# Optimization experiments

Measured on AMD Instinct MI355X. Metric: run time of the kernel, lower is better.

Reference implementation:

```python
import jax, jax.numpy as jnp
import numpy as np

N_NODES = 50000
N_EDGES = 400000
N_GRAPHS = 64
D_IN = 256
D_HID = 256
D_OUT = 16


def _gcn_conv(x, edge_index, W, b):
    """PyG-style GCNConv: h = D^{-1/2}(A+I)D^{-1/2} (x @ W) + b."""
    n = x.shape[0]
    loop = jnp.arange(n)
    src = jnp.concatenate([edge_index[0], loop])  # [E+N]
    dst = jnp.concatenate([edge_index[1], loop])
    deg = jax.ops.segment_sum(jnp.ones_like(dst, x.dtype), dst, num_segments=n)
    dinv = jnp.where(deg > 0, jax.lax.rsqrt(deg), jnp.zeros_like(deg))
    norm = dinv[src] * dinv[dst]  # [E+N]
    h = x @ W  # linear transform first (as PyG does)
    msg = h[src] * norm[:, None]  # gather + scale, [E+N, D]
    out = jax.ops.segment_sum(msg, dst, num_segments=n)  # scatter-add
    return out + b


def setup_inputs() -> dict:
    key = jax.random.key(0)
    ks = jax.random.split(key, 12)
    x = jax.random.normal(ks[0], (N_NODES, D_IN), dtype=jnp.float32)
    edge_index = jax.random.randint(ks[1], (2, N_EDGES), 0, N_NODES, dtype=jnp.int64)
    batch = jnp.sort(jax.random.randint(ks[2], (N_NODES,), 0, N_GRAPHS, dtype=jnp.int64))

    def glorot(k, fan_in, fan_out):
        s = np.sqrt(6.0 / (fan_in + fan_out)).astype(np.float32)
        return jax.random.uniform(k, (fan_in, fan_out), jnp.float32, -s, s)

    return {
        "x": x,
        "edge_index": edge_index,
        "batch": batch,
        "W1": glorot(ks[3], D_IN, D_HID), "b1": jnp.zeros((D_HID,), jnp.float32),
        "W2": glorot(ks[4], D_HID, D_HID), "b2": jnp.zeros((D_HID,), jnp.float32),
        "W3": glorot(ks[5], D_HID, D_HID), "b3": jnp.zeros((D_HID,), jnp.float32),
        "Wfc": glorot(ks[6], D_HID, D_OUT), "bfc": jnp.zeros((D_OUT,), jnp.float32),
    }


def reference(x, edge_index, batch, W1, b1, W2, b2, W3, b3, Wfc, bfc):
    h = jax.nn.relu(_gcn_conv(x, edge_index, W1, b1))
    h = jax.nn.relu(_gcn_conv(h, edge_index, W2, b2))
    h = jax.nn.relu(_gcn_conv(h, edge_index, W3, b3))
    # global_mean_pool over batch ids
    sums = jax.ops.segment_sum(h, batch, num_segments=N_GRAPHS)  # [G, D]
    cnts = jax.ops.segment_sum(jnp.ones_like(batch, h.dtype), batch, num_segments=N_GRAPHS)
    pooled = sums / jnp.maximum(cnts, 1.0)[:, None]
    return pooled @ Wfc + bfc  # [G, D_OUT]
```

## Files before the change

kernel.cpp:

```cpp
#include <hip/hip_runtime.h>

#define NN 50000
#define NE 400000
#define NG 64
#define D 256
#define DOUT 16

typedef __attribute__((ext_vector_type(8))) short bf16x8;
typedef __attribute__((ext_vector_type(4))) float f32x4;

__device__ __forceinline__ short f2bf(float x) {
    union { float f; unsigned u; } v; v.f = x;
    unsigned r = v.u + 0x7fffu + ((v.u >> 16) & 1u);
    return (short)(r >> 16);
}
__device__ __forceinline__ float bf2f(short h) {
    union { float f; unsigned u; } v;
    v.u = ((unsigned)(unsigned short)h) << 16;
    return v.f;
}

__device__ __forceinline__ void async_cp16(void* lds, const void* g) {
    __builtin_amdgcn_global_load_lds(
        (const __attribute__((address_space(1))) unsigned int*)g,
        (__attribute__((address_space(3))) unsigned int*)lds, 16, 0, 0);
}


__global__ void k_init(int* __restrict__ cnt, float* __restrict__ pooled,
                       const int* __restrict__ batch, float* __restrict__ inv_cnt,
                       int n) {
    int i = blockIdx.x * 256 + threadIdx.x;
    if (i < n) cnt[i] = 0;
    if (i < NG * D) pooled[i] = 0.f;
    if (blockIdx.x == 0 && threadIdx.x < NG) {
        int g = threadIdx.x;
        int lo = 0, hi = n;
        while (lo < hi) { int mid = (lo + hi) >> 1; if (batch[mid] < g) lo = mid + 1; else hi = mid; }
        int start = lo;
        hi = n;
        while (lo < hi) { int mid = (lo + hi) >> 1; if (batch[mid] < g + 1) lo = mid + 1; else hi = mid; }
        inv_cnt[g] = 1.f / fmaxf((float)(lo - start), 1.f);
    }
}

__global__ void k_count(const int* __restrict__ eidx, int* __restrict__ cnt, int E) {
    int e = blockIdx.x * blockDim.x + threadIdx.x;
    if (e < E) atomicAdd(&cnt[eidx[E + e]], 1);
}

__global__ void k_scan1(const int* __restrict__ cnt, int* __restrict__ excl,
                        int* __restrict__ bsums, float* __restrict__ dinv, int n) {
    __shared__ int sh[256];
    int tid = threadIdx.x;
    int base = blockIdx.x * 1024;
    int v[4]; int tsum = 0;
    for (int j = 0; j < 4; ++j) {
        int i = base + tid * 4 + j;
        v[j] = (i < n) ? cnt[i] : 0;
        if (i < n) dinv[i] = rsqrtf((float)(v[j] + 1));
        tsum += v[j];
    }
    sh[tid] = tsum; __syncthreads();
    for (int d = 1; d < 256; d <<= 1) {
        int t = (tid >= d) ? sh[tid - d] : 0;
        __syncthreads();
        sh[tid] += t;
        __syncthreads();
    }
    int run = sh[tid] - tsum;
    for (int j = 0; j < 4; ++j) {
        int i = base + tid * 4 + j;
        if (i < n) excl[i] = run;
        run += v[j];
    }
    if (tid == 255) bsums[blockIdx.x] = sh[255];
}

__global__ void k_scan2(int* bsums, int nb) {
    __shared__ int sh[64];
    int tid = threadIdx.x;
    int v = (tid < nb) ? bsums[tid] : 0;
    sh[tid] = v; __syncthreads();
    for (int d = 1; d < 64; d <<= 1) {
        int t = (tid >= d) ? sh[tid - d] : 0;
        __syncthreads();
        sh[tid] += t;
        __syncthreads();
    }
    if (tid < nb) bsums[tid] = sh[tid] - v;
}

__global__ void k_scan3(int* __restrict__ row_ptr, const int* __restrict__ bsums,
                        int* __restrict__ cursor, int n, int E) {
    int i = blockIdx.x * blockDim.x + threadIdx.x;
    if (i < n) {
        int v = row_ptr[i] + bsums[i >> 10];
        row_ptr[i] = v;
        cursor[i] = v;
    }
    if (i == 0) row_ptr[n] = E;
}

__global__ void k_fill(const int* __restrict__ eidx, int* __restrict__ cursor,
                       int* __restrict__ col_src, int E) {
    int e = blockIdx.x * blockDim.x + threadIdx.x;
    if (e < E) {
        int d = eidx[E + e];
        int pos = atomicAdd(&cursor[d], 1);
        col_src[pos] = eidx[e];
    }
}


__global__ void k_split(const float* __restrict__ x, unsigned short* __restrict__ ahi,
                        int total4, int xblocks,
                        const float* __restrict__ W1, short* __restrict__ w1hi, short* __restrict__ w1lo,
                        const float* __restrict__ W2, short* __restrict__ w2hi, short* __restrict__ w2lo,
                        const float* __restrict__ W3, short* __restrict__ w3hi, short* __restrict__ w3lo) {
    if (blockIdx.x < (unsigned)xblocks) {
        int i = blockIdx.x * 256 + threadIdx.x;
        if (i >= total4) return;
        float4 v = ((const float4*)x)[i];
        ushort4 h;
        h.x = (unsigned short)f2bf(v.x);
        h.y = (unsigned short)f2bf(v.y);
        h.z = (unsigned short)f2bf(v.z);
        h.w = (unsigned short)f2bf(v.w);
        ((ushort4*)ahi)[i] = h;
    } else {
        int wb = blockIdx.x - xblocks;
        int which = wb >> 8;
        int idx = (wb & 255) * 256 + threadIdx.x;
        int nn = idx >> 8, k = idx & 255;
        const float* W = (which == 0) ? W1 : (which == 1) ? W2 : W3;
        short* Whi = (which == 0) ? w1hi : (which == 1) ? w2hi : w3hi;
        short* Wlo = (which == 0) ? w1lo : (which == 1) ? w2lo : w3lo;
        float xv = W[k * 256 + nn];
        short h = f2bf(xv);
        Whi[idx] = h;
        Wlo[idx] = f2bf(xv - bf2f(h));
    }
}


__global__ __launch_bounds__(256) void k_gemm_mfma(
        const unsigned short* __restrict__ A,
        const short* __restrict__ Whi, const short* __restrict__ Wlo,
        const float* __restrict__ dinv, unsigned short* __restrict__ C, int M) {
    __shared__ short Ah_s[4096];
    __shared__ short Bh_s[4096];
    __shared__ short Bl_s[4096];

    const int tid = threadIdx.x;
    const int bm = blockIdx.x * 128;
    const int bn = blockIdx.y * 128;

    const int lane = tid & 63;
    const int w    = tid >> 6;
    const int wm   = w & 1;
    const int wn   = w >> 1;
    const int lm   = lane & 15;
    const int quad = lane >> 4;

    const int srow = tid >> 2, c = tid & 3;
    const int r0 = srow, r1 = 64 + srow;
    const int q0 = c ^ ((r0 >> 1) & 3);
    const int q1 = c ^ ((r1 >> 1) & 3);
    int ga0 = bm + r0; if (ga0 >= M) ga0 = M - 1;
    int ga1 = bm + r1; if (ga1 >= M) ga1 = M - 1;
    const unsigned short* pah0 = A + ((size_t)ga0 << 8) + q0 * 8;
    const unsigned short* pah1 = A + ((size_t)ga1 << 8) + q1 * 8;
    const short* pbh0 = Whi + ((size_t)(bn + r0) << 8) + q0 * 8;
    const short* pbh1 = Whi + ((size_t)(bn + r1) << 8) + q1 * 8;
    const short* pbl0 = Wlo + ((size_t)(bn + r0) << 8) + q0 * 8;
    const short* pbl1 = Wlo + ((size_t)(bn + r1) << 8) + q1 * 8;

    const int st0 = w * 512;
    const int st1 = 2048 + w * 512;

    int oa[4], ob[4];
    #pragma unroll
    for (int i = 0; i < 4; ++i) {
        int ra = wm * 64 + i * 16 + lm;
        oa[i] = ra * 32 + ((quad ^ ((ra >> 1) & 3)) * 8);
        int rb = wn * 64 + i * 16 + lm;
        ob[i] = rb * 32 + ((quad ^ ((rb >> 1) & 3)) * 8);
    }

    f32x4 acc[4][4];
    #pragma unroll
    for (int i = 0; i < 4; ++i)
        #pragma unroll
        for (int j = 0; j < 4; ++j)
            acc[i][j] = (f32x4){0.f, 0.f, 0.f, 0.f};

    for (int k0 = 0; k0 < D; k0 += 32) {
        async_cp16(&Ah_s[st0], pah0 + k0);
        async_cp16(&Ah_s[st1], pah1 + k0);
        async_cp16(&Bh_s[st0], pbh0 + k0);
        async_cp16(&Bh_s[st1], pbh1 + k0);
        async_cp16(&Bl_s[st0], pbl0 + k0);
        async_cp16(&Bl_s[st1], pbl1 + k0);
        __syncthreads();

        bf16x8 Ah[4], Bh[4], Bl[4];
        #pragma unroll
        for (int i = 0; i < 4; ++i) {
            Ah[i] = *(const bf16x8*)&Ah_s[oa[i]];
            Bh[i] = *(const bf16x8*)&Bh_s[ob[i]];
            Bl[i] = *(const bf16x8*)&Bl_s[ob[i]];
        }
        #pragma unroll
        for (int mi = 0; mi < 4; ++mi)
            #pragma unroll
            for (int ni = 0; ni < 4; ++ni) {
                acc[mi][ni] = __builtin_amdgcn_mfma_f32_16x16x32_bf16(Ah[mi], Bh[ni], acc[mi][ni], 0, 0, 0);
                acc[mi][ni] = __builtin_amdgcn_mfma_f32_16x16x32_bf16(Ah[mi], Bl[ni], acc[mi][ni], 0, 0, 0);
            }
        __syncthreads();
    }

    #pragma unroll
    for (int mi = 0; mi < 4; ++mi) {
        int rbase = bm + wm * 64 + mi * 16 + quad * 4;
        #pragma unroll
        for (int r = 0; r < 4; ++r) {
            int grow = rbase + r;
            if (grow < M) {
                float s = dinv[grow];
                #pragma unroll
                for (int ni = 0; ni < 4; ++ni) {
                    int col = bn + wn * 64 + ni * 16 + lm;
                    C[(size_t)grow * D + col] = (unsigned short)f2bf(acc[mi][ni][r] * s);
                }
            }
        }
    }
}


__global__ __launch_bounds__(256) void k_agg(
        const unsigned short* __restrict__ h, const float* __restrict__ dinv,
        const int* __restrict__ row_ptr, const int* __restrict__ col_src,
        const float* __restrict__ bias,
        unsigned short* __restrict__ ohi, int n) {
    int w = threadIdx.x >> 6, lane = threadIdx.x & 63;
    int n0 = blockIdx.x * 8 + w * 2;
    if (n0 >= n) return;
    int n1 = n0 + 1;
    bool has1 = n1 < n;

    float di0 = dinv[n0];
    float di1 = has1 ? dinv[n1] : 0.f;
    ushort4 s0 = ((const ushort4*)(h + (size_t)n0 * D))[lane];
    float4 a0 = make_float4(bf2f(s0.x), bf2f(s0.y), bf2f(s0.z), bf2f(s0.w));
    float4 a1 = make_float4(0.f, 0.f, 0.f, 0.f);
    if (has1) {
        ushort4 s1 = ((const ushort4*)(h + (size_t)n1 * D))[lane];
        a1 = make_float4(bf2f(s1.x), bf2f(s1.y), bf2f(s1.z), bf2f(s1.w));
    }

    int c0 = row_ptr[n0], e0 = row_ptr[n0 + 1];
    int c1 = e0, e1 = has1 ? row_ptr[n1 + 1] : e0;

    while (c0 < e0 || c1 < e1) {
        int cnt0 = min(64, e0 - c0); if (cnt0 < 0) cnt0 = 0;
        int cnt1 = min(64, e1 - c1); if (cnt1 < 0) cnt1 = 0;
        int i0 = (lane < cnt0) ? col_src[c0 + lane] : 0;
        int i1 = (lane < cnt1) ? col_src[c1 + lane] : 0;
        int m = max(cnt0, cnt1);
        for (int e = 0; e < m; e += 8) {
            int k0 = cnt0 - e;
            int k1 = cnt1 - e;
            ushort4 u0[8], u1[8];
            #pragma unroll
            for (int j = 0; j < 8; ++j)
                if (j < k0) {
                    int s = __shfl(i0, e + j);
                    u0[j] = ((const ushort4*)(h + (size_t)s * D))[lane];
                }
            #pragma unroll
            for (int j = 0; j < 8; ++j)
                if (j < k1) {
                    int s = __shfl(i1, e + j);
                    u1[j] = ((const ushort4*)(h + (size_t)s * D))[lane];
                }
            #pragma unroll
            for (int j = 0; j < 8; ++j)
                if (j < k0) {
                    a0.x += bf2f(u0[j].x); a0.y += bf2f(u0[j].y);
                    a0.z += bf2f(u0[j].z); a0.w += bf2f(u0[j].w);
                }
            #pragma unroll
            for (int j = 0; j < 8; ++j)
                if (j < k1) {
                    a1.x += bf2f(u1[j].x); a1.y += bf2f(u1[j].y);
                    a1.z += bf2f(u1[j].z); a1.w += bf2f(u1[j].w);
                }
        }
        c0 += cnt0; c1 += cnt1;
    }

    float4 b = ((const float4*)bias)[lane];
    ushort4 o0;
    o0.x = (unsigned short)f2bf(fmaxf(a0.x * di0 + b.x, 0.f));
    o0.y = (unsigned short)f2bf(fmaxf(a0.y * di0 + b.y, 0.f));
    o0.z = (unsigned short)f2bf(fmaxf(a0.z * di0 + b.z, 0.f));
    o0.w = (unsigned short)f2bf(fmaxf(a0.w * di0 + b.w, 0.f));
    ((ushort4*)(ohi + (size_t)n0 * D))[lane] = o0;
    if (has1) {
        ushort4 o1;
        o1.x = (unsigned short)f2bf(fmaxf(a1.x * di1 + b.x, 0.f));
        o1.y = (unsigned short)f2bf(fmaxf(a1.y * di1 + b.y, 0.f));
        o1.z = (unsigned short)f2bf(fmaxf(a1.z * di1 + b.z, 0.f));
        o1.w = (unsigned short)f2bf(fmaxf(a1.w * di1 + b.w, 0.f));
        ((ushort4*)(ohi + (size_t)n1 * D))[lane] = o1;
    }
}


__global__ __launch_bounds__(256) void k_pool_sum(
        const unsigned short* __restrict__ hi,
        const int* __restrict__ batch, float* __restrict__ pooled, int n) {
    int beg = blockIdx.x * 64;
    if (beg >= n) return;
    int end = min(beg + 64, n);
    int t = threadIdx.x;
    float acc = 0.f;
    int cur = batch[beg];
    for (int i = beg; i < end; ++i) {
        int g = batch[i];
        if (g != cur) {
            atomicAdd(&pooled[cur * D + t], acc);
            acc = 0.f;
            cur = g;
        }
        acc += bf2f(hi[(size_t)i * D + t]);
    }
    atomicAdd(&pooled[cur * D + t], acc);
}


__global__ void k_fc(const float* __restrict__ pooled, const float* __restrict__ inv_cnt,
                     const float* __restrict__ W, const float* __restrict__ b,
                     float* __restrict__ out) {
    int t = blockIdx.x * blockDim.x + threadIdx.x;
    if (t >= NG * DOUT) return;
    int g = t >> 4, o = t & 15;
    float acc = 0.f;
    for (int k = 0; k < D; ++k) acc += pooled[g * D + k] * W[k * DOUT + o];
    out[t] = acc * inv_cnt[g] + b[o];
}


extern "C" void kernel_launch(void* const* d_in, const int* in_sizes, int n_in,
                              void* d_out, int out_size, void* d_ws, size_t ws_size,
                              hipStream_t stream) {
    const float* x    = (const float*)d_in[0];
    const int*   eidx = (const int*)d_in[1];
    const int*   batch= (const int*)d_in[2];
    const float* W1   = (const float*)d_in[3];
    const float* b1   = (const float*)d_in[4];
    const float* W2   = (const float*)d_in[5];
    const float* b2   = (const float*)d_in[6];
    const float* W3   = (const float*)d_in[7];
    const float* b3   = (const float*)d_in[8];
    const float* Wfc  = (const float*)d_in[9];
    const float* bfc  = (const float*)d_in[10];
    float* out = (float*)d_out;

    const int n = in_sizes[0] / D;
    const int E = in_sizes[1] / 2;

    char* p = (char*)d_ws;
    auto take = [&](size_t bytes) -> void* {
        void* q = (void*)p;
        p += (bytes + 255) & ~(size_t)255;
        return q;
    };
    int*   cnt     = (int*)take((size_t)n * 4);
    int*   row_ptr = (int*)take((size_t)(n + 1) * 4);
    int*   cursor  = (int*)take((size_t)n * 4);
    int*   col_src = (int*)take((size_t)E * 4);
    int*   bsums   = (int*)take(256 * 4);
    float* dinv    = (float*)take((size_t)n * 4);
    float* inv_cnt = (float*)take((size_t)NG * 4);
    short* w1hi    = (short*)take((size_t)D * D * 2);
    short* w1lo    = (short*)take((size_t)D * D * 2);
    short* w2hi    = (short*)take((size_t)D * D * 2);
    short* w2lo    = (short*)take((size_t)D * D * 2);
    short* w3hi    = (short*)take((size_t)D * D * 2);
    short* w3lo    = (short*)take((size_t)D * D * 2);
    unsigned short* hbuf = (unsigned short*)take((size_t)n * D * 2);
    unsigned short* ahi  = (unsigned short*)take((size_t)n * D * 2);
    float* pooled  = (float*)take((size_t)NG * D * 4);

    int tb = 256;
    int gn = (n + tb - 1) / tb;
    int ge = (E + tb - 1) / tb;
    int nb = (n + 1023) / 1024;
    int total4 = n * D / 4;
    int xblocks = (total4 + 255) / 256;

    k_init<<<gn, tb, 0, stream>>>(cnt, pooled, batch, inv_cnt, n);
    k_split<<<xblocks + 3 * 256, tb, 0, stream>>>(x, ahi, total4, xblocks,
                                                  W1, w1hi, w1lo, W2, w2hi, w2lo, W3, w3hi, w3lo);
    k_count<<<ge, tb, 0, stream>>>(eidx, cnt, E);
    k_scan1<<<nb, 256, 0, stream>>>(cnt, row_ptr, bsums, dinv, n);
    k_scan2<<<1, 64, 0, stream>>>(bsums, nb);
    k_scan3<<<gn, tb, 0, stream>>>(row_ptr, bsums, cursor, n, E);
    k_fill<<<ge, tb, 0, stream>>>(eidx, cursor, col_src, E);

    dim3 ggrid((n + 127) / 128, 2);
    int agrid = (n + 7) / 8;

    k_gemm_mfma<<<ggrid, 256, 0, stream>>>(ahi, w1hi, w1lo, dinv, hbuf, n);
    k_agg<<<agrid, 256, 0, stream>>>(hbuf, dinv, row_ptr, col_src, b1, ahi, n);

    k_gemm_mfma<<<ggrid, 256, 0, stream>>>(ahi, w2hi, w2lo, dinv, hbuf, n);
    k_agg<<<agrid, 256, 0, stream>>>(hbuf, dinv, row_ptr, col_src, b2, ahi, n);

    k_gemm_mfma<<<ggrid, 256, 0, stream>>>(ahi, w3hi, w3lo, dinv, hbuf, n);
    k_agg<<<agrid, 256, 0, stream>>>(hbuf, dinv, row_ptr, col_src, b3, ahi, n);

    k_pool_sum<<<(n + 63) / 64, 256, 0, stream>>>(ahi, batch, pooled, n);
    k_fc<<<4, 256, 0, stream>>>(pooled, inv_cnt, Wfc, bfc, out);
}
```

Baseline: 410.1 us.

## Widen GEMM tile to full N and fuse mean-pool into last aggregation

The GEMM now computes all 256 output columns per block, so each A tile is loaded once instead of twice. This doubles B shared memory and the accumulator registers and sets launch bounds for two blocks per CU. The third aggregation kernel now reduces its ReLU outputs per graph through LDS and atomics into the pooled buffer. That removes the bf16 write of the final layer's activations and the separate pooling pass. In exchange there are more atomics, and register pressure may lower occupancy or cause spills.

```diff
diff --git a/kernel.cpp b/kernel.cpp
--- a/kernel.cpp
+++ b/kernel.cpp
@@ -144,17 +144,16 @@
 }
 
 
-__global__ __launch_bounds__(256) void k_gemm_mfma(
+__global__ __launch_bounds__(256, 2) void k_gemm_mfma(
         const unsigned short* __restrict__ A,
         const short* __restrict__ Whi, const short* __restrict__ Wlo,
         const float* __restrict__ dinv, unsigned short* __restrict__ C, int M) {
     __shared__ short Ah_s[4096];
-    __shared__ short Bh_s[4096];
-    __shared__ short Bl_s[4096];
+    __shared__ short Bh_s[8192];
+    __shared__ short Bl_s[8192];
 
     const int tid = threadIdx.x;
     const int bm = blockIdx.x * 128;
-    const int bn = blockIdx.y * 128;
 
     const int lane = tid & 63;
     const int w    = tid >> 6;
@@ -164,57 +163,64 @@
     const int quad = lane >> 4;
 
     const int srow = tid >> 2, c = tid & 3;
-    const int r0 = srow, r1 = 64 + srow;
-    const int q0 = c ^ ((r0 >> 1) & 3);
-    const int q1 = c ^ ((r1 >> 1) & 3);
-    int ga0 = bm + r0; if (ga0 >= M) ga0 = M - 1;
-    int ga1 = bm + r1; if (ga1 >= M) ga1 = M - 1;
-    const unsigned short* pah0 = A + ((size_t)ga0 << 8) + q0 * 8;
-    const unsigned short* pah1 = A + ((size_t)ga1 << 8) + q1 * 8;
-    const short* pbh0 = Whi + ((size_t)(bn + r0) << 8) + q0 * 8;
-    const short* pbh1 = Whi + ((size_t)(bn + r1) << 8) + q1 * 8;
-    const short* pbl0 = Wlo + ((size_t)(bn + r0) << 8) + q0 * 8;
-    const short* pbl1 = Wlo + ((size_t)(bn + r1) << 8) + q1 * 8;
-
-    const int st0 = w * 512;
-    const int st1 = 2048 + w * 512;
-
-    int oa[4], ob[4];
+    const int q = c ^ ((srow >> 1) & 3);
+    int ga0 = bm + srow;        if (ga0 >= M) ga0 = M - 1;
+    int ga1 = bm + 64 + srow;   if (ga1 >= M) ga1 = M - 1;
+    const unsigned short* pa0 = A + ((size_t)ga0 << 8) + q * 8;
+    const unsigned short* pa1 = A + ((size_t)ga1 << 8) + q * 8;
+    const short* pbh[4]; const short* pbl[4];
+    #pragma unroll
+    for (int j = 0; j < 4; ++j) {
+        pbh[j] = Whi + ((size_t)(j * 64 + srow) << 8) + q * 8;
+        pbl[j] = Wlo + ((size_t)(j * 64 + srow) << 8) + q * 8;
+    }
+
+    const int stA0 = w * 512, stA1 = 2048 + w * 512;
+    int stB[4];
+    #pragma unroll
+    for (int j = 0; j < 4; ++j) stB[j] = j * 2048 + w * 512;
+
+    int oa[4], ob[8];
     #pragma unroll
     for (int i = 0; i < 4; ++i) {
         int ra = wm * 64 + i * 16 + lm;
         oa[i] = ra * 32 + ((quad ^ ((ra >> 1) & 3)) * 8);
-        int rb = wn * 64 + i * 16 + lm;
+    }
+    #pragma unroll
+    for (int i = 0; i < 8; ++i) {
+        int rb = wn * 128 + i * 16 + lm;
         ob[i] = rb * 32 + ((quad ^ ((rb >> 1) & 3)) * 8);
     }
 
-    f32x4 acc[4][4];
+    f32x4 acc[4][8];
     #pragma unroll
     for (int i = 0; i < 4; ++i)
         #pragma unroll
-        for (int j = 0; j < 4; ++j)
+        for (int j = 0; j < 8; ++j)
             acc[i][j] = (f32x4){0.f, 0.f, 0.f, 0.f};
 
     for (int k0 = 0; k0 < D; k0 += 32) {
-        async_cp16(&Ah_s[st0], pah0 + k0);
-        async_cp16(&Ah_s[st1], pah1 + k0);
-        async_cp16(&Bh_s[st0], pbh0 + k0);
-        async_cp16(&Bh_s[st1], pbh1 + k0);
-        async_cp16(&Bl_s[st0], pbl0 + k0);
-        async_cp16(&Bl_s[st1], pbl1 + k0);
-        __syncthreads();
-
-        bf16x8 Ah[4], Bh[4], Bl[4];
-        #pragma unroll
-        for (int i = 0; i < 4; ++i) {
-            Ah[i] = *(const bf16x8*)&Ah_s[oa[i]];
+        async_cp16(&Ah_s[stA0], pa0 + k0);
+        async_cp16(&Ah_s[stA1], pa1 + k0);
+        #pragma unroll
+        for (int j = 0; j < 4; ++j) {
+            async_cp16(&Bh_s[stB[j]], pbh[j] + k0);
+            async_cp16(&Bl_s[stB[j]], pbl[j] + k0);
+        }
+        __syncthreads();
+
+        bf16x8 Ah[4], Bh[8], Bl[8];
+        #pragma unroll
+        for (int i = 0; i < 4; ++i) Ah[i] = *(const bf16x8*)&Ah_s[oa[i]];
+        #pragma unroll
+        for (int i = 0; i < 8; ++i) {
             Bh[i] = *(const bf16x8*)&Bh_s[ob[i]];
             Bl[i] = *(const bf16x8*)&Bl_s[ob[i]];
         }
         #pragma unroll
         for (int mi = 0; mi < 4; ++mi)
             #pragma unroll
-            for (int ni = 0; ni < 4; ++ni) {
+            for (int ni = 0; ni < 8; ++ni) {
                 acc[mi][ni] = __builtin_amdgcn_mfma_f32_16x16x32_bf16(Ah[mi], Bh[ni], acc[mi][ni], 0, 0, 0);
                 acc[mi][ni] = __builtin_amdgcn_mfma_f32_16x16x32_bf16(Ah[mi], Bl[ni], acc[mi][ni], 0, 0, 0);
             }
@@ -230,8 +236,8 @@
             if (grow < M) {
                 float s = dinv[grow];
                 #pragma unroll
-                for (int ni = 0; ni < 4; ++ni) {
-                    int col = bn + wn * 64 + ni * 16 + lm;
+                for (int ni = 0; ni < 8; ++ni) {
+                    int col = wn * 128 + ni * 16 + lm;
                     C[(size_t)grow * D + col] = (unsigned short)f2bf(acc[mi][ni][r] * s);
                 }
             }
@@ -240,27 +246,17 @@
 }
 
 
-__global__ __launch_bounds__(256) void k_agg(
-        const unsigned short* __restrict__ h, const float* __restrict__ dinv,
-        const int* __restrict__ row_ptr, const int* __restrict__ col_src,
-        const float* __restrict__ bias,
-        unsigned short* __restrict__ ohi, int n) {
-    int w = threadIdx.x >> 6, lane = threadIdx.x & 63;
-    int n0 = blockIdx.x * 8 + w * 2;
-    if (n0 >= n) return;
-    int n1 = n0 + 1;
-    bool has1 = n1 < n;
-
-    float di0 = dinv[n0];
-    float di1 = has1 ? dinv[n1] : 0.f;
+__device__ __forceinline__ void agg_two(
+        const unsigned short* __restrict__ h, const int* __restrict__ row_ptr,
+        const int* __restrict__ col_src, int n0, int n1, bool has1, int lane,
+        float4& a0, float4& a1) {
     ushort4 s0 = ((const ushort4*)(h + (size_t)n0 * D))[lane];
-    float4 a0 = make_float4(bf2f(s0.x), bf2f(s0.y), bf2f(s0.z), bf2f(s0.w));
-    float4 a1 = make_float4(0.f, 0.f, 0.f, 0.f);
+    a0 = make_float4(bf2f(s0.x), bf2f(s0.y), bf2f(s0.z), bf2f(s0.w));
+    a1 = make_float4(0.f, 0.f, 0.f, 0.f);
     if (has1) {
         ushort4 s1 = ((const ushort4*)(h + (size_t)n1 * D))[lane];
         a1 = make_float4(bf2f(s1.x), bf2f(s1.y), bf2f(s1.z), bf2f(s1.w));
     }
-
     int c0 = row_ptr[n0], e0 = row_ptr[n0 + 1];
     int c1 = e0, e1 = has1 ? row_ptr[n1 + 1] : e0;
 
@@ -301,7 +297,22 @@
         }
         c0 += cnt0; c1 += cnt1;
     }
-
+}
+
+__global__ __launch_bounds__(256) void k_agg(
+        const unsigned short* __restrict__ h, const float* __restrict__ dinv,
+        const int* __restrict__ row_ptr, const int* __restrict__ col_src,
+        const float* __restrict__ bias,
+        unsigned short* __restrict__ ohi, int n) {
+    int w = threadIdx.x >> 6, lane = threadIdx.x & 63;
+    int n0 = blockIdx.x * 8 + w * 2;
+    if (n0 >= n) return;
+    int n1 = n0 + 1;
+    bool has1 = n1 < n;
+    float4 a0, a1;
+    agg_two(h, row_ptr, col_src, n0, n1, has1, lane, a0, a1);
+
+    float di0 = dinv[n0];
     float4 b = ((const float4*)bias)[lane];
     ushort4 o0;
     o0.x = (unsigned short)f2bf(fmaxf(a0.x * di0 + b.x, 0.f));
@@ -310,6 +321,7 @@
     o0.w = (unsigned short)f2bf(fmaxf(a0.w * di0 + b.w, 0.f));
     ((ushort4*)(ohi + (size_t)n0 * D))[lane] = o0;
     if (has1) {
+        float di1 = dinv[n1];
         ushort4 o1;
         o1.x = (unsigned short)f2bf(fmaxf(a1.x * di1 + b.x, 0.f));
         o1.y = (unsigned short)f2bf(fmaxf(a1.y * di1 + b.y, 0.f));
@@ -319,26 +331,83 @@
     }
 }
 
-
-__global__ __launch_bounds__(256) void k_pool_sum(
-        const unsigned short* __restrict__ hi,
-        const int* __restrict__ batch, float* __restrict__ pooled, int n) {
-    int beg = blockIdx.x * 64;
-    if (beg >= n) return;
-    int end = min(beg + 64, n);
-    int t = threadIdx.x;
-    float acc = 0.f;
-    int cur = batch[beg];
-    for (int i = beg; i < end; ++i) {
-        int g = batch[i];
-        if (g != cur) {
-            atomicAdd(&pooled[cur * D + t], acc);
-            acc = 0.f;
-            cur = g;
-        }
-        acc += bf2f(hi[(size_t)i * D + t]);
-    }
-    atomicAdd(&pooled[cur * D + t], acc);
+__global__ __launch_bounds__(256) void k_agg3(
+        const unsigned short* __restrict__ h, const float* __restrict__ dinv,
+        const int* __restrict__ row_ptr, const int* __restrict__ col_src,
+        const float* __restrict__ bias, const int* __restrict__ batch,
+        float* __restrict__ pooled, int n) {
+    __shared__ float sred[4][256];
+    int w = threadIdx.x >> 6, lane = threadIdx.x & 63;
+    int nb0 = blockIdx.x * 8;
+    int nb1 = min(nb0 + 7, n - 1);
+    bool uni = (batch[nb0] == batch[nb1]);
+
+    int n0 = nb0 + w * 2;
+    int n1 = n0 + 1;
+    bool act = n0 < n;
+    bool has1 = n1 < n;
+
+    float4 r0 = make_float4(0.f, 0.f, 0.f, 0.f);
+    float4 r1 = make_float4(0.f, 0.f, 0.f, 0.f);
+    int g0 = 0, g1 = 0;
+    if (act) {
+        float4 a0, a1;
+        agg_two(h, row_ptr, col_src, n0, n1, has1, lane, a0, a1);
+        float di0 = dinv[n0];
+        float4 b = ((const float4*)bias)[lane];
+        r0.x = fmaxf(a0.x * di0 + b.x, 0.f);
+        r0.y = fmaxf(a0.y * di0 + b.y, 0.f);
+        r0.z = fmaxf(a0.z * di0 + b.z, 0.f);
+        r0.w = fmaxf(a0.w * di0 + b.w, 0.f);
+        g0 = batch[n0];
+        if (has1) {
+            float di1 = dinv[n1];
+            r1.x = fmaxf(a1.x * di1 + b.x, 0.f);
+            r1.y = fmaxf(a1.y * di1 + b.y, 0.f);
+            r1.z = fmaxf(a1.z * di1 + b.z, 0.f);
+            r1.w = fmaxf(a1.w * di1 + b.w, 0.f);
+            g1 = batch[n1];
+        }
+    }
+
+    if (uni) {
+        float4 ws = make_float4(r0.x + r1.x, r0.y + r1.y, r0.z + r1.z, r0.w + r1.w);
+        ((float4*)&sred[w][lane * 4])[0] = ws;
+        __syncthreads();
+        if (w == 0) {
+            float4 t0 = ((const float4*)&sred[0][lane * 4])[0];
+            float4 t1 = ((const float4*)&sred[1][lane * 4])[0];
+            float4 t2 = ((const float4*)&sred[2][lane * 4])[0];
+            float4 t3 = ((const float4*)&sred[3][lane * 4])[0];
+            int g = batch[nb0];
+            float* pg = pooled + g * D + lane * 4;
+            atomicAdd(pg + 0, t0.x + t1.x + t2.x + t3.x);
+            atomicAdd(pg + 1, t0.y + t1.y + t2.y + t3.y);
+            atomicAdd(pg + 2, t0.z + t1.z + t2.z + t3.z);
+            atomicAdd(pg + 3, t0.w + t1.w + t2.w + t3.w);
+        }
+    } else if (act) {
+        if (has1 && g1 == g0) {
+            float* pg = pooled + g0 * D + lane * 4;
+            atomicAdd(pg + 0, r0.x + r1.x);
+            atomicAdd(pg + 1, r0.y + r1.y);
+            atomicAdd(pg + 2, r0.z + r1.z);
+            atomicAdd(pg + 3, r0.w + r1.w);
+        } else {
+            float* pg = pooled + g0 * D + lane * 4;
+            atomicAdd(pg + 0, r0.x);
+            atomicAdd(pg + 1, r0.y);
+            atomicAdd(pg + 2, r0.z);
+            atomicAdd(pg + 3, r0.w);
+            if (has1) {
+                float* pg1 = pooled + g1 * D + lane * 4;
+                atomicAdd(pg1 + 0, r1.x);
+                atomicAdd(pg1 + 1, r1.y);
+                atomicAdd(pg1 + 2, r1.z);
+                atomicAdd(pg1 + 3, r1.w);
+            }
+        }
+    }
 }
 
 
@@ -412,7 +481,7 @@
     k_scan3<<<gn, tb, 0, stream>>>(row_ptr, bsums, cursor, n, E);
     k_fill<<<ge, tb, 0, stream>>>(eidx, cursor, col_src, E);
 
-    dim3 ggrid((n + 127) / 128, 2);
+    int ggrid = (n + 127) / 128;
     int agrid = (n + 7) / 8;
 
     k_gemm_mfma<<<ggrid, 256, 0, stream>>>(ahi, w1hi, w1lo, dinv, hbuf, n);
@@ -422,8 +491,7 @@
     k_agg<<<agrid, 256, 0, stream>>>(hbuf, dinv, row_ptr, col_src, b2, ahi, n);
 
     k_gemm_mfma<<<ggrid, 256, 0, stream>>>(ahi, w3hi, w3lo, dinv, hbuf, n);
-    k_agg<<<agrid, 256, 0, stream>>>(hbuf, dinv, row_ptr, col_src, b3, ahi, n);
-
-    k_pool_sum<<<(n + 63) / 64, 256, 0, stream>>>(ahi, batch, pooled, n);
+    k_agg3<<<agrid, 256, 0, stream>>>(hbuf, dinv, row_ptr, col_src, b3, batch, pooled, n);
+
     k_fc<<<4, 256, 0, stream>>>(pooled, inv_cnt, Wfc, bfc, out);
 }
```

Result: no change. 404.9 us (-1.3%).
